# Performance work log

Hardware: AMD Instinct MI355X
Metric: run time of the kernel (lower is better)

The kernel has to match this reference:

```python
import jax, jax.numpy as jnp
import numpy as np

BATCH = 16384
N_FEATURES = 768
FT_OUT = 1024
ACTIVE_P = 32.0 / 768.0  # ~32 active features per board, like real positions


def setup_inputs() -> dict:
    key = jax.random.key(0)
    k1, k2, k3, k4, k5, k6 = jax.random.split(key, 6)
    # densified sparse one-hot boards: binary {0,1} with ~32/768 density
    board_stm = (jax.random.uniform(k1, (BATCH, N_FEATURES)) < ACTIVE_P).astype(jnp.float32)
    board_nstm = (jax.random.uniform(k2, (BATCH, N_FEATURES)) < ACTIVE_P).astype(jnp.float32)
    # Linear(768, FT_OUT): weight [out, in], bias [out]
    W_ft = jax.random.normal(k3, (FT_OUT, N_FEATURES), dtype=jnp.float32) * (1.0 / np.sqrt(N_FEATURES))
    b_ft = jax.random.normal(k4, (FT_OUT,), dtype=jnp.float32) * 0.01
    # Linear(2*FT_OUT, 1)
    W_out = jax.random.normal(k5, (1, 2 * FT_OUT), dtype=jnp.float32) * (1.0 / np.sqrt(2 * FT_OUT))
    b_out = jax.random.normal(k6, (1,), dtype=jnp.float32) * 0.01
    return {"board_stm": board_stm, "board_nstm": board_nstm,
            "W_ft": W_ft, "b_ft": b_ft, "W_out": W_out, "b_out": b_out}


def screlu(x):
    # SCReLU: clamp(x, 0, 1)^2
    return jnp.square(jnp.clip(x, 0.0, 1.0))


def reference(board_stm, board_nstm, W_ft, b_ft, W_out, b_out):
    # feature transformer applied to both perspectives (shared weights)
    stm = jnp.einsum('bf,of->bo', board_stm, W_ft) + b_ft   # [B, FT_OUT]
    nstm = jnp.einsum('bf,of->bo', board_nstm, W_ft) + b_ft  # [B, FT_OUT]
    hidden = screlu(jnp.concatenate([stm, nstm], axis=1))    # [B, 2*FT_OUT]
    out = jnp.einsum('bh,oh->bo', hidden, W_out) + b_out     # [B, 1]
    return jax.nn.sigmoid(out)
```

## Files before the change

### kernel.cpp

```cpp
#include <hip/hip_runtime.h>
#include <stdint.h>

#define BATCH 16384
#define NF 768
#define FT 1024
#define RB 32
#define GR (2 * RB)
#define THREADS 1024
#define NW 16
#define ALD 784
#define NKS 12

typedef int i32x4 __attribute__((ext_vector_type(4)));

__global__ __launch_bounds__(192) void prep_wq(const float* __restrict__ W_ft,
                                               char* __restrict__ Wq,
                                               float* __restrict__ invs) {
    const int o = blockIdx.x;
    const int t = threadIdx.x;
    __shared__ float smax[3];
    __shared__ float sscale;
    const float4 v = *(const float4*)(W_ft + (size_t)o * NF + t * 4);
    float m = fmaxf(fmaxf(fabsf(v.x), fabsf(v.y)), fmaxf(fabsf(v.z), fabsf(v.w)));
    #pragma unroll
    for (int s = 32; s > 0; s >>= 1) m = fmaxf(m, __shfl_down(m, s, 64));
    if ((t & 63) == 0) smax[t >> 6] = m;
    __syncthreads();
    if (t == 0) {
        const float am = fmaxf(fmaxf(smax[0], smax[1]), smax[2]);
        sscale = 127.0f / am;
        invs[o] = am / 127.0f;
    }
    __syncthreads();
    const float s = sscale;
    const float arr[4] = {v.x, v.y, v.z, v.w};
    uint32_t pk = 0;
    #pragma unroll
    for (int j = 0; j < 4; ++j) {
        const int q = (int)rintf(arr[j] * s);
        pk |= ((uint32_t)(unsigned char)(char)q) << (8 * j);
    }
    *(uint32_t*)(Wq + (size_t)o * NF + t * 4) = pk;
}

__device__ __forceinline__ uint32_t pack01(float4 v) {
    return (uint32_t)(v.x != 0.0f) | ((uint32_t)(v.y != 0.0f) << 8)
         | ((uint32_t)(v.z != 0.0f) << 16) | ((uint32_t)(v.w != 0.0f) << 24);
}

__global__ __launch_bounds__(THREADS, 4) void nnue_mfma(
    const float* __restrict__ bstm, const float* __restrict__ bnstm,
    const char* __restrict__ Wq, const float* __restrict__ invs,
    const float* __restrict__ b_ft, const float* __restrict__ W_out,
    const float* __restrict__ b_out, float* __restrict__ out)
{
    __shared__ __align__(16) char Albs[GR * ALD];
    __shared__ float red[GR][NW];

    const int t = threadIdx.x;
    const int w = t >> 6;
    const int l = t & 63;
    const int b0 = blockIdx.x * RB;

    float4 sv[12];
    int srow[12], sc4[12];
    #pragma unroll
    for (int it = 0; it < 12; ++it) {
        const int g = it * THREADS + t;
        const int row = g / 192;
        const int c4 = g - row * 192;
        const float* src = (row < RB) ? (bstm + (size_t)(b0 + row) * NF)
                                      : (bnstm + (size_t)(b0 + row - RB) * NF);
        sv[it] = *(const float4*)(src + c4 * 4);
        srow[it] = row; sc4[it] = c4;
    }
    #pragma unroll
    for (int it = 0; it < 12; ++it)
        *(uint32_t*)(&Albs[srow[it] * ALD + sc4[it] * 4]) = pack01(sv[it]);
    __syncthreads();

    const int cl = l & 15;
    const int q = l >> 4;
    const char* bptr = Wq + (size_t)(w * 64 + cl) * NF + q * 16;
    const int aoff = cl * ALD + q * 16;

    i32x4 acc[4][4] = {};
    #pragma unroll 2
    for (int ks = 0; ks < NKS; ++ks) {
        i32x4 bfrag[4];
        #pragma unroll
        for (int c = 0; c < 4; ++c)
            bfrag[c] = *(const i32x4*)(bptr + (size_t)c * 16 * NF + ks * 64);
        i32x4 afrag[4];
        #pragma unroll
        for (int r = 0; r < 4; ++r)
            afrag[r] = *(const i32x4*)(&Albs[aoff + r * 16 * ALD + ks * 64]);
        #pragma unroll
        for (int r = 0; r < 4; ++r)
            #pragma unroll
            for (int c = 0; c < 4; ++c)
                acc[r][c] = __builtin_amdgcn_mfma_i32_16x16x64_i8(
                    afrag[r], bfrag[c], acc[r][c], 0, 0, 0);
    }

    float ps[4][4] = {};
    #pragma unroll
    for (int c = 0; c < 4; ++c) {
        const int col = w * 64 + c * 16 + cl;
        const float iv = invs[col];
        const float bf = b_ft[col];
        const float wo0 = W_out[col];
        const float wo1 = W_out[FT + col];
        #pragma unroll
        for (int r = 0; r < 4; ++r) {
            const float wo = (r < 2) ? wo0 : wo1;
            #pragma unroll
            for (int j = 0; j < 4; ++j) {
                float h = fmaf((float)acc[r][c][j], iv, bf);
                h = fminf(fmaxf(h, 0.0f), 1.0f);
                ps[r][j] = fmaf(h * h, wo, ps[r][j]);
            }
        }
    }
    #pragma unroll
    for (int r = 0; r < 4; ++r)
        #pragma unroll
        for (int j = 0; j < 4; ++j) {
            float v = ps[r][j];
            v += __shfl_xor(v, 1, 64);
            v += __shfl_xor(v, 2, 64);
            v += __shfl_xor(v, 4, 64);
            v += __shfl_xor(v, 8, 64);
            if (cl == 0) red[16 * r + 4 * q + j][w] = v;
        }
    __syncthreads();

    if (t < RB) {
        float x = b_out[0];
        #pragma unroll
        for (int w2 = 0; w2 < NW; ++w2)
            x += red[t][w2] + red[RB + t][w2];
        out[b0 + t] = 1.0f / (1.0f + expf(-x));
    }
}

extern "C" void kernel_launch(void* const* d_in, const int* in_sizes, int n_in,
                              void* d_out, int out_size, void* d_ws, size_t ws_size,
                              hipStream_t stream) {
    const float* board_stm  = (const float*)d_in[0];
    const float* board_nstm = (const float*)d_in[1];
    const float* W_ft       = (const float*)d_in[2];
    const float* b_ft       = (const float*)d_in[3];
    const float* W_out      = (const float*)d_in[4];
    const float* b_out      = (const float*)d_in[5];
    float* out = (float*)d_out;

    char* Wq = (char*)d_ws;
    float* invs = (float*)((char*)d_ws + (size_t)FT * NF);

    prep_wq<<<FT, 192, 0, stream>>>(W_ft, Wq, invs);
    nnue_mfma<<<BATCH / RB, THREADS, 0, stream>>>(board_stm, board_nstm, Wq, invs,
                                                  b_ft, W_out, b_out, out);
}
```

Baseline: 75.06 us.

## Pre-convert boards to int8 in separate kernels before MFMA kernel

Adds a conv_boards kernel that packs the fp32 one-hot boards into int8 bytes in workspace. The main MFMA kernel then loads 16-byte int8 chunks straight into LDS instead of loading float4s and packing them in place. The aim is to cut register and instruction cost of the staging phase. In exchange it adds two launches plus an extra write and reread of the int8 boards, and it only runs when the workspace is large enough. It also adds a sched_barrier between loads and LDS stores.

```diff
diff --git a/kernel.cpp b/kernel.cpp
--- a/kernel.cpp
+++ b/kernel.cpp
@@ -48,8 +48,22 @@
          | ((uint32_t)(v.z != 0.0f) << 16) | ((uint32_t)(v.w != 0.0f) << 24);
 }
 
+__global__ __launch_bounds__(256) void conv_boards(const float* __restrict__ src,
+                                                   unsigned char* __restrict__ dst,
+                                                   int n16) {
+    for (int i = blockIdx.x * 256 + threadIdx.x; i < n16; i += gridDim.x * 256) {
+        const float4* s = (const float4*)src + (size_t)i * 4;
+        const float4 a = s[0], b = s[1], c = s[2], d = s[3];
+        uint4 o;
+        o.x = pack01(a); o.y = pack01(b); o.z = pack01(c); o.w = pack01(d);
+        *(uint4*)(dst + (size_t)i * 16) = o;
+    }
+}
+
+template <bool PRE8>
 __global__ __launch_bounds__(THREADS, 4) void nnue_mfma(
     const float* __restrict__ bstm, const float* __restrict__ bnstm,
+    const unsigned char* __restrict__ a8s, const unsigned char* __restrict__ a8n,
     const char* __restrict__ Wq, const float* __restrict__ invs,
     const float* __restrict__ b_ft, const float* __restrict__ W_out,
     const float* __restrict__ b_out, float* __restrict__ out)
@@ -62,21 +76,38 @@
     const int l = t & 63;
     const int b0 = blockIdx.x * RB;
 
-    float4 sv[12];
-    int srow[12], sc4[12];
-    #pragma unroll
-    for (int it = 0; it < 12; ++it) {
-        const int g = it * THREADS + t;
-        const int row = g / 192;
-        const int c4 = g - row * 192;
-        const float* src = (row < RB) ? (bstm + (size_t)(b0 + row) * NF)
-                                      : (bnstm + (size_t)(b0 + row - RB) * NF);
-        sv[it] = *(const float4*)(src + c4 * 4);
-        srow[it] = row; sc4[it] = c4;
-    }
-    #pragma unroll
-    for (int it = 0; it < 12; ++it)
-        *(uint32_t*)(&Albs[srow[it] * ALD + sc4[it] * 4]) = pack01(sv[it]);
+    if (PRE8) {
+        uint4 v[3]; int row[3], c16[3];
+        #pragma unroll
+        for (int it = 0; it < 3; ++it) {
+            const int g = it * THREADS + t;
+            row[it] = g / 48; c16[it] = g - row[it] * 48;
+            const unsigned char* src = (row[it] < RB)
+                ? (a8s + (size_t)(b0 + row[it]) * NF)
+                : (a8n + (size_t)(b0 + row[it] - RB) * NF);
+            v[it] = *(const uint4*)(src + c16[it] * 16);
+        }
+        __builtin_amdgcn_sched_barrier(0);
+        #pragma unroll
+        for (int it = 0; it < 3; ++it)
+            *(uint4*)(&Albs[row[it] * ALD + c16[it] * 16]) = v[it];
+    } else {
+        float4 sv[12]; int srow[12], sc4[12];
+        #pragma unroll
+        for (int it = 0; it < 12; ++it) {
+            const int g = it * THREADS + t;
+            const int row = g / 192;
+            const int c4 = g - row * 192;
+            const float* src = (row < RB) ? (bstm + (size_t)(b0 + row) * NF)
+                                          : (bnstm + (size_t)(b0 + row - RB) * NF);
+            sv[it] = *(const float4*)(src + c4 * 4);
+            srow[it] = row; sc4[it] = c4;
+        }
+        __builtin_amdgcn_sched_barrier(0);
+        #pragma unroll
+        for (int it = 0; it < 12; ++it)
+            *(uint32_t*)(&Albs[srow[it] * ALD + sc4[it] * 4]) = pack01(sv[it]);
+    }
     __syncthreads();
 
     const int cl = l & 15;
@@ -157,8 +188,19 @@
 
     char* Wq = (char*)d_ws;
     float* invs = (float*)((char*)d_ws + (size_t)FT * NF);
+    unsigned char* a8s = (unsigned char*)d_ws + (size_t)FT * NF + 4096;
+    unsigned char* a8n = a8s + (size_t)BATCH * NF;
+    const size_t needed = (size_t)FT * NF + 4096 + 2 * (size_t)BATCH * NF;
 
     prep_wq<<<FT, 192, 0, stream>>>(W_ft, Wq, invs);
-    nnue_mfma<<<BATCH / RB, THREADS, 0, stream>>>(board_stm, board_nstm, Wq, invs,
-                                                  b_ft, W_out, b_out, out);
-}
+    if (ws_size >= needed) {
+        const int n16 = BATCH * NF / 16;
+        conv_boards<<<1536, 256, 0, stream>>>(board_stm, a8s, n16);
+        conv_boards<<<1536, 256, 0, stream>>>(board_nstm, a8n, n16);
+        nnue_mfma<true><<<BATCH / RB, THREADS, 0, stream>>>(
+            board_stm, board_nstm, a8s, a8n, Wq, invs, b_ft, W_out, b_out, out);
+    } else {
+        nnue_mfma<false><<<BATCH / RB, THREADS, 0, stream>>>(
+            board_stm, board_nstm, a8s, a8n, Wq, invs, b_ft, W_out, b_out, out);
+    }
+}
```

After: 89.80 us. 19.6% more time.

## Pre-pack boards into MFMA fragment layout and double-buffer weight fragments

Applied to the files above, without the earlier changes.

Adds a separate kernel that converts the float boards to int8 and writes them into a per-block layout that matches the MFMA A-fragment order. The main kernel can then copy that buffer straight into LDS and read conflict-free fragments. The K loop is restructured to double-buffer the B fragments from global memory, with s_setprio around the MFMA groups, and launch bounds change from 4 to 2 waves per SIMD. The cost is an extra kernel launch plus a round trip of the packed boards through global memory, and the original path remains only as a fallback when the workspace is too small.

```diff
diff --git a/kernel.cpp b/kernel.cpp
--- a/kernel.cpp
+++ b/kernel.cpp
@@ -5,11 +5,11 @@
 #define NF 768
 #define FT 1024
 #define RB 32
-#define GR (2 * RB)
+#define GR 64
 #define THREADS 1024
 #define NW 16
-#define ALD 784
 #define NKS 12
+#define ABLK (NKS * 4 * 64 * 16)
 
 typedef int i32x4 __attribute__((ext_vector_type(4)));
 
@@ -48,13 +48,41 @@
          | ((uint32_t)(v.z != 0.0f) << 16) | ((uint32_t)(v.w != 0.0f) << 24);
 }
 
-__global__ __launch_bounds__(THREADS, 4) void nnue_mfma(
+__device__ __forceinline__ int frag_slot(int row, int c16) {
+    const int r = row >> 4, cl = row & 15;
+    const int ks = c16 >> 2, q = c16 & 3;
+    return ((ks * 4 + r) << 6) + q * 16 + cl;
+}
+
+__global__ __launch_bounds__(256) void conv_boards(const float* __restrict__ bstm,
+                                                   const float* __restrict__ bnstm,
+                                                   unsigned char* __restrict__ a8f) {
+    const int NCH = BATCH * 48;
+    for (int g = blockIdx.x * 256 + threadIdx.x; g < 2 * NCH; g += gridDim.x * 256) {
+        const int p = (g >= NCH);
+        const int gg = p ? g - NCH : g;
+        const int brow = gg / 48;
+        const int c16 = gg - brow * 48;
+        const float4* src = (const float4*)((p ? bnstm : bstm)
+                                            + (size_t)brow * NF + c16 * 16);
+        uint4 o;
+        o.x = pack01(src[0]); o.y = pack01(src[1]);
+        o.z = pack01(src[2]); o.w = pack01(src[3]);
+        const int blk = brow >> 5;
+        const int row = (p << 5) | (brow & 31);
+        *(uint4*)(a8f + (size_t)blk * ABLK + ((size_t)frag_slot(row, c16) << 4)) = o;
+    }
+}
+
+template <bool PRE8>
+__global__ __launch_bounds__(THREADS, 2) void nnue_mfma(
     const float* __restrict__ bstm, const float* __restrict__ bnstm,
+    const unsigned char* __restrict__ a8f,
     const char* __restrict__ Wq, const float* __restrict__ invs,
     const float* __restrict__ b_ft, const float* __restrict__ W_out,
     const float* __restrict__ b_out, float* __restrict__ out)
 {
-    __shared__ __align__(16) char Albs[GR * ALD];
+    __shared__ __align__(16) char Albs[ABLK];
     __shared__ float red[GR][NW];
 
     const int t = threadIdx.x;
@@ -62,47 +90,72 @@
     const int l = t & 63;
     const int b0 = blockIdx.x * RB;
 
-    float4 sv[12];
-    int srow[12], sc4[12];
-    #pragma unroll
-    for (int it = 0; it < 12; ++it) {
-        const int g = it * THREADS + t;
-        const int row = g / 192;
-        const int c4 = g - row * 192;
-        const float* src = (row < RB) ? (bstm + (size_t)(b0 + row) * NF)
-                                      : (bnstm + (size_t)(b0 + row - RB) * NF);
-        sv[it] = *(const float4*)(src + c4 * 4);
-        srow[it] = row; sc4[it] = c4;
-    }
-    #pragma unroll
-    for (int it = 0; it < 12; ++it)
-        *(uint32_t*)(&Albs[srow[it] * ALD + sc4[it] * 4]) = pack01(sv[it]);
+    if (PRE8) {
+        const uint4* src = (const uint4*)(a8f + (size_t)blockIdx.x * ABLK);
+        uint4* dst = (uint4*)Albs;
+        const uint4 v0 = src[t], v1 = src[1024 + t], v2 = src[2048 + t];
+        dst[t] = v0; dst[1024 + t] = v1; dst[2048 + t] = v2;
+    } else {
+        #pragma unroll
+        for (int it = 0; it < 3; ++it) {
+            const int c = it * 1024 + t;
+            const int row = c / 48;
+            const int c16 = c - row * 48;
+            const float4* s = (const float4*)(((row < RB)
+                ? (bstm + (size_t)(b0 + row) * NF)
+                : (bnstm + (size_t)(b0 + row - RB) * NF)) + c16 * 16);
+            uint4 o;
+            o.x = pack01(s[0]); o.y = pack01(s[1]);
+            o.z = pack01(s[2]); o.w = pack01(s[3]);
+            *(uint4*)(Albs + ((size_t)frag_slot(row, c16) << 4)) = o;
+        }
+    }
     __syncthreads();
 
     const int cl = l & 15;
-    const int q = l >> 4;
-    const char* bptr = Wq + (size_t)(w * 64 + cl) * NF + q * 16;
-    const int aoff = cl * ALD + q * 16;
+    const char* bp = Wq + (size_t)(w * 64 + cl) * NF + (l >> 4) * 16;
+    const i32x4* af = (const i32x4*)Albs;
+
+    i32x4 be[4], bo[4];
+    #pragma unroll
+    for (int c = 0; c < 4; ++c)
+        be[c] = *(const i32x4*)(bp + (size_t)c * 16 * NF);
 
     i32x4 acc[4][4] = {};
-    #pragma unroll 2
-    for (int ks = 0; ks < NKS; ++ks) {
-        i32x4 bfrag[4];
+    #pragma unroll
+    for (int kk = 0; kk < 6; ++kk) {
+        const int ks0 = 2 * kk, ks1 = 2 * kk + 1;
         #pragma unroll
         for (int c = 0; c < 4; ++c)
-            bfrag[c] = *(const i32x4*)(bptr + (size_t)c * 16 * NF + ks * 64);
-        i32x4 afrag[4];
-        #pragma unroll
-        for (int r = 0; r < 4; ++r)
-            afrag[r] = *(const i32x4*)(&Albs[aoff + r * 16 * ALD + ks * 64]);
-        #pragma unroll
-        for (int r = 0; r < 4; ++r)
+            bo[c] = *(const i32x4*)(bp + (size_t)c * 16 * NF + ks1 * 64);
+        __builtin_amdgcn_s_setprio(1);
+        #pragma unroll
+        for (int r = 0; r < 4; ++r) {
+            const i32x4 a = af[(ks0 * 4 + r) * 64 + l];
             #pragma unroll
             for (int c = 0; c < 4; ++c)
                 acc[r][c] = __builtin_amdgcn_mfma_i32_16x16x64_i8(
-                    afrag[r], bfrag[c], acc[r][c], 0, 0, 0);
-    }
-
+                    a, be[c], acc[r][c], 0, 0, 0);
+        }
+        __builtin_amdgcn_s_setprio(0);
+        if (kk < 5) {
+            #pragma unroll
+            for (int c = 0; c < 4; ++c)
+                be[c] = *(const i32x4*)(bp + (size_t)c * 16 * NF + (ks1 + 1) * 64);
+        }
+        __builtin_amdgcn_s_setprio(1);
+        #pragma unroll
+        for (int r = 0; r < 4; ++r) {
+            const i32x4 a = af[(ks1 * 4 + r) * 64 + l];
+            #pragma unroll
+            for (int c = 0; c < 4; ++c)
+                acc[r][c] = __builtin_amdgcn_mfma_i32_16x16x64_i8(
+                    a, bo[c], acc[r][c], 0, 0, 0);
+        }
+        __builtin_amdgcn_s_setprio(0);
+    }
+
+    const int q = l >> 4;
     float ps[4][4] = {};
     #pragma unroll
     for (int c = 0; c < 4; ++c) {
@@ -157,8 +210,16 @@
 
     char* Wq = (char*)d_ws;
     float* invs = (float*)((char*)d_ws + (size_t)FT * NF);
+    unsigned char* a8f = (unsigned char*)d_ws + (size_t)FT * NF + 4096;
+    const size_t needed = (size_t)FT * NF + 4096 + (size_t)(BATCH / RB) * ABLK;
 
     prep_wq<<<FT, 192, 0, stream>>>(W_ft, Wq, invs);
-    nnue_mfma<<<BATCH / RB, THREADS, 0, stream>>>(board_stm, board_nstm, Wq, invs,
-                                                  b_ft, W_out, b_out, out);
-}
+    if (ws_size >= needed) {
+        conv_boards<<<2048, 256, 0, stream>>>(board_stm, board_nstm, a8f);
+        nnue_mfma<true><<<BATCH / RB, THREADS, 0, stream>>>(
+            board_stm, board_nstm, a8f, Wq, invs, b_ft, W_out, b_out, out);
+    } else {
+        nnue_mfma<false><<<BATCH / RB, THREADS, 0, stream>>>(
+            board_stm, board_nstm, a8f, Wq, invs, b_ft, W_out, b_out, out);
+    }
+}
```

After: 86.31 us. +15.0%, slower.

## Restructure MFMA kernel into 256-thread blocks looping over output column chunks

Applied to the files above, without the earlier changes.

Each block now uses 4 waves instead of 16 and loops over four 256-column chunks, so every wave reuses the same LDS board tile across more output columns. The packed 0/1 board tile is stored in LDS in MFMA-fragment order, which makes the A-fragment reads conflict-free and contiguous and drops the padded row layout. Weight fragments for the next K step are prefetched into registers, and the MFMA section runs at raised wave priority. Fewer waves per block and more registers per thread may reduce how well memory latency is hidden.

```diff
diff --git a/kernel.cpp b/kernel.cpp
--- a/kernel.cpp
+++ b/kernel.cpp
@@ -4,12 +4,11 @@
 #define BATCH 16384
 #define NF 768
 #define FT 1024
-#define RB 32
-#define GR (2 * RB)
-#define THREADS 1024
-#define NW 16
-#define ALD 784
+#define RBB 32
+#define GR 64
+#define THREADS 256
 #define NKS 12
+#define ABLK (NKS * 4 * 64 * 16)
 
 typedef int i32x4 __attribute__((ext_vector_type(4)));
 
@@ -48,80 +47,119 @@
          | ((uint32_t)(v.z != 0.0f) << 16) | ((uint32_t)(v.w != 0.0f) << 24);
 }
 
-__global__ __launch_bounds__(THREADS, 4) void nnue_mfma(
+__global__ __launch_bounds__(THREADS, 2) void nnue_mfma(
     const float* __restrict__ bstm, const float* __restrict__ bnstm,
     const char* __restrict__ Wq, const float* __restrict__ invs,
     const float* __restrict__ b_ft, const float* __restrict__ W_out,
     const float* __restrict__ b_out, float* __restrict__ out)
 {
-    __shared__ __align__(16) char Albs[GR * ALD];
-    __shared__ float red[GR][NW];
+    __shared__ __align__(16) char Albs[ABLK];
+    __shared__ float red[GR][4];
 
     const int t = threadIdx.x;
     const int w = t >> 6;
     const int l = t & 63;
-    const int b0 = blockIdx.x * RB;
-
-    float4 sv[12];
-    int srow[12], sc4[12];
-    #pragma unroll
-    for (int it = 0; it < 12; ++it) {
-        const int g = it * THREADS + t;
-        const int row = g / 192;
-        const int c4 = g - row * 192;
-        const float* src = (row < RB) ? (bstm + (size_t)(b0 + row) * NF)
-                                      : (bnstm + (size_t)(b0 + row - RB) * NF);
-        sv[it] = *(const float4*)(src + c4 * 4);
-        srow[it] = row; sc4[it] = c4;
-    }
-    #pragma unroll
-    for (int it = 0; it < 12; ++it)
-        *(uint32_t*)(&Albs[srow[it] * ALD + sc4[it] * 4]) = pack01(sv[it]);
+    const int b0 = blockIdx.x * RBB;
+
+    #pragma unroll
+    for (int bt = 0; bt < 3; ++bt) {
+        float4 v[16];
+        int rows[4], c16s[4];
+        #pragma unroll
+        for (int u = 0; u < 4; ++u) {
+            const int chunkid = (bt * 4 + u) * THREADS + t;
+            const int row = chunkid / 48;
+            const int c16 = chunkid - row * 48;
+            rows[u] = row; c16s[u] = c16;
+            const float* src = ((row < RBB)
+                ? (bstm + (size_t)(b0 + row) * NF)
+                : (bnstm + (size_t)(b0 + row - RBB) * NF)) + c16 * 16;
+            #pragma unroll
+            for (int k = 0; k < 4; ++k)
+                v[u * 4 + k] = *(const float4*)(src + k * 4);
+        }
+        __builtin_amdgcn_sched_barrier(0);
+        #pragma unroll
+        for (int u = 0; u < 4; ++u) {
+            const int row = rows[u], c16 = c16s[u];
+            const int r = row >> 4, cl2 = row & 15;
+            const int ks = c16 >> 2, qq = c16 & 3;
+            uint4 o;
+            o.x = pack01(v[u * 4 + 0]); o.y = pack01(v[u * 4 + 1]);
+            o.z = pack01(v[u * 4 + 2]); o.w = pack01(v[u * 4 + 3]);
+            const int slot = ((ks * 4 + r) << 6) + (qq << 4) + cl2;
+            *(uint4*)(&Albs[(size_t)slot << 4]) = o;
+        }
+    }
     __syncthreads();
 
     const int cl = l & 15;
     const int q = l >> 4;
-    const char* bptr = Wq + (size_t)(w * 64 + cl) * NF + q * 16;
-    const int aoff = cl * ALD + q * 16;
-
-    i32x4 acc[4][4] = {};
-    #pragma unroll 2
-    for (int ks = 0; ks < NKS; ++ks) {
-        i32x4 bfrag[4];
+    const i32x4* af = (const i32x4*)Albs;
+    float ps[4][4] = {};
+
+    #pragma unroll
+    for (int ch = 0; ch < 4; ++ch) {
+        const int colbase = ch * 256 + w * 64;
+        const char* bp = Wq + (size_t)(colbase + cl) * NF + q * 16;
+
+        i32x4 bcur[4];
         #pragma unroll
         for (int c = 0; c < 4; ++c)
-            bfrag[c] = *(const i32x4*)(bptr + (size_t)c * 16 * NF + ks * 64);
-        i32x4 afrag[4];
+            bcur[c] = *(const i32x4*)(bp + (size_t)c * 16 * NF);
+
+        float iv[4], bf[4], wos[4], won[4];
+        #pragma unroll
+        for (int c = 0; c < 4; ++c) {
+            const int col = colbase + c * 16 + cl;
+            iv[c] = invs[col]; bf[c] = b_ft[col];
+            wos[c] = W_out[col]; won[c] = W_out[FT + col];
+        }
+
+        i32x4 acc[4][4];
         #pragma unroll
         for (int r = 0; r < 4; ++r)
-            afrag[r] = *(const i32x4*)(&Albs[aoff + r * 16 * ALD + ks * 64]);
-        #pragma unroll
-        for (int r = 0; r < 4; ++r)
             #pragma unroll
             for (int c = 0; c < 4; ++c)
-                acc[r][c] = __builtin_amdgcn_mfma_i32_16x16x64_i8(
-                    afrag[r], bfrag[c], acc[r][c], 0, 0, 0);
-    }
-
-    float ps[4][4] = {};
-    #pragma unroll
-    for (int c = 0; c < 4; ++c) {
-        const int col = w * 64 + c * 16 + cl;
-        const float iv = invs[col];
-        const float bf = b_ft[col];
-        const float wo0 = W_out[col];
-        const float wo1 = W_out[FT + col];
-        #pragma unroll
-        for (int r = 0; r < 4; ++r) {
-            const float wo = (r < 2) ? wo0 : wo1;
-            #pragma unroll
-            for (int j = 0; j < 4; ++j) {
-                float h = fmaf((float)acc[r][c][j], iv, bf);
-                h = fminf(fmaxf(h, 0.0f), 1.0f);
-                ps[r][j] = fmaf(h * h, wo, ps[r][j]);
+                acc[r][c] = (i32x4){0, 0, 0, 0};
+
+        #pragma unroll
+        for (int ks = 0; ks < NKS; ++ks) {
+            i32x4 bnxt[4];
+            if (ks < NKS - 1) {
+                #pragma unroll
+                for (int c = 0; c < 4; ++c)
+                    bnxt[c] = *(const i32x4*)(bp + (size_t)c * 16 * NF + (ks + 1) * 64);
             }
-        }
-    }
+            __builtin_amdgcn_s_setprio(1);
+            #pragma unroll
+            for (int r = 0; r < 4; ++r) {
+                const i32x4 a = af[(ks * 4 + r) * 64 + l];
+                #pragma unroll
+                for (int c = 0; c < 4; ++c)
+                    acc[r][c] = __builtin_amdgcn_mfma_i32_16x16x64_i8(
+                        a, bcur[c], acc[r][c], 0, 0, 0);
+            }
+            __builtin_amdgcn_s_setprio(0);
+            #pragma unroll
+            for (int c = 0; c < 4; ++c) bcur[c] = bnxt[c];
+        }
+
+        #pragma unroll
+        for (int c = 0; c < 4; ++c) {
+            #pragma unroll
+            for (int r = 0; r < 4; ++r) {
+                const float wo = (r < 2) ? wos[c] : won[c];
+                #pragma unroll
+                for (int j = 0; j < 4; ++j) {
+                    float h = fmaf((float)acc[r][c][j], iv[c], bf[c]);
+                    h = fminf(fmaxf(h, 0.0f), 1.0f);
+                    ps[r][j] = fmaf(h * h, wo, ps[r][j]);
+                }
+            }
+        }
+    }
+
     #pragma unroll
     for (int r = 0; r < 4; ++r)
         #pragma unroll
@@ -135,11 +173,11 @@
         }
     __syncthreads();
 
-    if (t < RB) {
+    if (t < RBB) {
         float x = b_out[0];
         #pragma unroll
-        for (int w2 = 0; w2 < NW; ++w2)
-            x += red[t][w2] + red[RB + t][w2];
+        for (int w2 = 0; w2 < 4; ++w2)
+            x += red[t][w2] + red[RBB + t][w2];
         out[b0 + t] = 1.0f / (1.0f + expf(-x));
     }
 }
@@ -159,6 +197,6 @@
     float* invs = (float*)((char*)d_ws + (size_t)FT * NF);
 
     prep_wq<<<FT, 192, 0, stream>>>(W_ft, Wq, invs);
-    nnue_mfma<<<BATCH / RB, THREADS, 0, stream>>>(board_stm, board_nstm, Wq, invs,
-                                                  b_ft, W_out, b_out, out);
-}
+    nnue_mfma<<<BATCH / RBB, THREADS, 0, stream>>>(
+        board_stm, board_nstm, Wq, invs, b_ft, W_out, b_out, out);
+}
```

New measurement: 89.33 us. 1.19x slower.
